# Kernel optimization log

Hardware: AMD Instinct MI355X
Metric: run time of the kernel (lower is better)

Reference implementation:

```python
import jax, jax.numpy as jnp
import numpy as np

S, D, H, L, FF = 4096, 128, 4, 3, 1024
DH = D // H
LN_EPS = 1e-5


def _layernorm(x, g, b):
    m = jnp.mean(x, axis=-1, keepdims=True)
    v = jnp.mean((x - m) ** 2, axis=-1, keepdims=True)
    return (x - m) * jax.lax.rsqrt(v + LN_EPS) * g + b


def setup_inputs() -> dict:
    key = jax.random.key(0)
    ks = jax.random.split(key, 16)
    w = lambda k, shp, s=0.05: jax.random.normal(k, shp, dtype=jnp.float32) * s
    return {
        "src": jax.random.normal(ks[0], (S, 1, D), dtype=jnp.float32),
        # per-layer transformer params, stacked on leading L axis
        "Wqkv": w(ks[1], (L, 3 * D, D)),
        "bqkv": jnp.zeros((L, 3 * D), jnp.float32),
        "Wo": w(ks[2], (L, D, D)),
        "bo": jnp.zeros((L, D), jnp.float32),
        "ln1_g": jnp.ones((L, D), jnp.float32),
        "ln1_b": jnp.zeros((L, D), jnp.float32),
        "W1": w(ks[3], (L, FF, D)),
        "b1": jnp.zeros((L, FF), jnp.float32),
        "W2": w(ks[4], (L, D, FF)),
        "b2": jnp.zeros((L, D), jnp.float32),
        "ln2_g": jnp.ones((L, D), jnp.float32),
        "ln2_b": jnp.zeros((L, D), jnp.float32),
        "fc1_W": w(ks[5], (D, D)),
        "fc1_b": jnp.zeros((D,), jnp.float32),
        "fc2_W": w(ks[6], (D, D)),
        "fc2_b": jnp.zeros((D,), jnp.float32),
    }


def reference(src, Wqkv, bqkv, Wo, bo, ln1_g, ln1_b, W1, b1, W2, b2,
              ln2_g, ln2_b, fc1_W, fc1_b, fc2_W, fc2_b):
    x = src[:, 0, :]  # [S, D] (batch=1, squeezed as in the torch module)
    scale = 1.0 / np.sqrt(DH).astype(np.float32)
    for l in range(L):  # small fixed layer count
        # --- self-attention (post-norm, as in torch TransformerEncoderLayer, eval mode) ---
        qkv = x @ Wqkv[l].T + bqkv[l]                      # [S, 3D]
        q, k, v = jnp.split(qkv, 3, axis=-1)
        q = q.reshape(S, H, DH)
        k = k.reshape(S, H, DH)
        v = v.reshape(S, H, DH)
        att = jax.nn.softmax(jnp.einsum('shd,thd->hst', q, k) * scale, axis=-1)
        o = jnp.einsum('hst,thd->shd', att, v).reshape(S, D)
        o = o @ Wo[l].T + bo[l]
        x = _layernorm(x + o, ln1_g[l], ln1_b[l])
        # --- feed-forward ---
        f = jax.nn.relu(x @ W1[l].T + b1[l]) @ W2[l].T + b2[l]
        x = _layernorm(x + f, ln2_g[l], ln2_b[l])
    # head
    x = jax.nn.relu(x @ fc1_W.T + fc1_b)
    x = x @ fc2_W.T + fc2_b
    # pairwise cosine similarity, clamped at min 1e-6 (vectorized form of pCosineSim)
    xn = x / jnp.linalg.norm(x, axis=1, keepdims=True)
    return jnp.maximum(xn @ xn.T, 1e-6)
```

## Files before the change

kernel.cpp:

```cpp
#include <hip/hip_runtime.h>
#include <math.h>

#define S 4096
#define QK_SCALE 0.17677669529663687f
#define LOG2E    1.44269504088896f
#define SPLIT 8
#define KS (S / SPLIT)

typedef _Float16 f16x8 __attribute__((ext_vector_type(8)));
typedef _Float16 f16x4 __attribute__((ext_vector_type(4)));
typedef _Float16 f16x2 __attribute__((ext_vector_type(2)));
typedef float f32x4 __attribute__((ext_vector_type(4)));

template<int R>
__device__ __forceinline__ void stageT(_Float16 (*dst)[136], const _Float16* __restrict__ src,
                                       int ld, int row0, int col0, int tid) {
    int r = tid >> 4, cb = (tid & 15) * 8;
#pragma unroll
    for (int v = 0; v < R / 16; v++)
        *(f16x8*)&dst[v * 16 + r][cb] =
            *(const f16x8*)(src + (size_t)(row0 + v * 16 + r) * ld + col0 + cb);
}

__global__ __launch_bounds__(256) void setup_cvt(const float* __restrict__ q,
                                                 const float* __restrict__ wo,
                                                 const float* __restrict__ w1,
                                                 const float* __restrict__ w2,
                                                 const float* __restrict__ f1,
                                                 const float* __restrict__ f2,
                                                 _Float16* __restrict__ dst,
                                                 const float* __restrict__ a,
                                                 float* __restrict__ x,
                                                 _Float16* __restrict__ xh)
{
    int bb = blockIdx.x;
    if (bb < 992) {
        const float* src; size_t dof; int lb;
        if (bb < 144)      { src = q;  dof = 0;      lb = bb; }
        else if (bb < 192) { src = wo; dof = 147456; lb = bb - 144; }
        else if (bb < 576) { src = w1; dof = 196608; lb = bb - 192; }
        else if (bb < 960) { src = w2; dof = 589824; lb = bb - 576; }
        else if (bb < 976) { src = f1; dof = 983040; lb = bb - 960; }
        else               { src = f2; dof = 999424; lb = bb - 976; }
        int i = lb * 1024 + threadIdx.x * 4;
        float4 v = *(const float4*)(src + i);
        f16x4 h = {(_Float16)v.x, (_Float16)v.y, (_Float16)v.z, (_Float16)v.w};
        *(f16x4*)(dst + dof + i) = h;
    } else {
        int i = (bb - 992) * 256 + threadIdx.x;
        float4 v = ((const float4*)a)[i];
        ((float4*)x)[i] = v;
        f16x4 h = {(_Float16)v.x, (_Float16)v.y, (_Float16)v.z, (_Float16)v.w};
        ((f16x4*)xh)[i] = h;
    }
}

__global__ __launch_bounds__(256) void gemm_qkv(const _Float16* __restrict__ xh,
                                                const _Float16* __restrict__ Wh,
                                                const float* __restrict__ bias,
                                                _Float16* __restrict__ qh,
                                                _Float16* __restrict__ kh,
                                                _Float16* __restrict__ vt)
{
    __shared__ _Float16 Ah[16][136], Bh[128][136];
    int tid = threadIdx.x, w = tid >> 6, l = tid & 63, lc = l & 15, lr = l >> 4;
    int m0 = blockIdx.x * 16, by = blockIdx.y;

    stageT<16>(Ah, xh, 128, m0, 0, tid);
    stageT<128>(Bh, Wh, 128, by * 128, 0, tid);
    __syncthreads();

    f32x4 acc[2];
#pragma unroll
    for (int j = 0; j < 2; j++) acc[j] = {0.f, 0.f, 0.f, 0.f};
#pragma unroll
    for (int ks = 0; ks < 4; ks++) {
        f16x8 af = *(const f16x8*)&Ah[lc][ks * 32 + lr * 8];
#pragma unroll
        for (int j = 0; j < 2; j++) {
            f16x8 bf = *(const f16x8*)&Bh[w * 32 + j * 16 + lc][ks * 32 + lr * 8];
            acc[j] = __builtin_amdgcn_mfma_f32_16x16x32_f16(af, bf, acc[j], 0, 0, 0);
        }
    }

    int mb = m0 + lr * 4;
#pragma unroll
    for (int j = 0; j < 2; j++) {
        int n = w * 32 + j * 16 + lc;
        float bb = bias[by * 128 + n];
        if (by == 0) {
#pragma unroll
            for (int r = 0; r < 4; r++)
                qh[(size_t)(mb + r) * 128 + n] =
                    (_Float16)((acc[j][r] + bb) * (QK_SCALE * LOG2E));
        } else if (by == 1) {
            int hh = n >> 5, d = n & 31;
#pragma unroll
            for (int r = 0; r < 4; r++)
                kh[((size_t)hh * S + mb + r) * 32 + d] = (_Float16)(acc[j][r] + bb);
        } else {
            f16x4 pk;
#pragma unroll
            for (int r = 0; r < 4; r++) pk[r] = (_Float16)(acc[j][r] + bb);
            *(f16x4*)&vt[(size_t)n * S + mb] = pk;
        }
    }
}

__global__ __launch_bounds__(256) void attn_mfma(const _Float16* __restrict__ qh,
                                                 const _Float16* __restrict__ kh,
                                                 const _Float16* __restrict__ vt,
                                                 _Float16* __restrict__ part,
                                                 float* __restrict__ mll)
{
    __shared__ _Float16 Ks[2][64][32];
    __shared__ _Float16 Vt[2][32][72];
    __shared__ _Float16 Ps[4][16][72];
    int h = blockIdx.y, q0 = blockIdx.x * 64, z = blockIdx.z;
    int tid = threadIdx.x;
    int w = tid >> 6, l = tid & 63;
    int lc = l & 15, lr = l >> 4;

    f16x8 qf = *(const f16x8*)&qh[(size_t)(q0 + w * 16 + lc) * 128 + h * 32 + lr * 8];

    const _Float16* khh = kh + (size_t)h * S * 32;
    const _Float16* vth = vt + (size_t)h * 32 * S;

    int krow = tid >> 2, kcol = (tid & 3) * 8;
    int vrow = tid >> 3, vcol = (tid & 7) * 8;

    f32x4 o0 = {0.f, 0.f, 0.f, 0.f}, o1 = {0.f, 0.f, 0.f, 0.f};
    float lp = 0.f;

    int k0 = z * KS;
    {
        f16x8 kr = *(const f16x8*)&khh[(size_t)(k0 + krow) * 32 + kcol];
        f16x8 vr = *(const f16x8*)&vth[(size_t)vrow * S + k0 + vcol];
        *(f16x8*)&Ks[0][krow][kcol] = kr;
        *(f16x8*)&Vt[0][vrow][vcol] = vr;
    }
    __syncthreads();

    int cur = 0;
#pragma unroll 1
    for (int t8 = 0; t8 < KS / 64; t8++) {
        bool more = (t8 + 1 < KS / 64);
        f16x8 kr, vr;
        if (more) {
            int kn = k0 + (t8 + 1) * 64;
            kr = *(const f16x8*)&khh[(size_t)(kn + krow) * 32 + kcol];
            vr = *(const f16x8*)&vth[(size_t)vrow * S + kn + vcol];
        }

        f32x4 st[4];
#pragma unroll
        for (int t = 0; t < 4; t++) {
            f16x8 kf = *(const f16x8*)&Ks[cur][t * 16 + lc][lr * 8];
            f32x4 zz = {0.f, 0.f, 0.f, 0.f};
            st[t] = __builtin_amdgcn_mfma_f32_16x16x32_f16(kf, qf, zz, 0, 0, 0);
        }
#pragma unroll
        for (int t = 0; t < 4; t++) {
            float p0 = exp2f(st[t][0]), p1 = exp2f(st[t][1]);
            float p2 = exp2f(st[t][2]), p3 = exp2f(st[t][3]);
            lp += (p0 + p1) + (p2 + p3);
            f16x2 h0 = {(_Float16)p0, (_Float16)p1};
            f16x2 h1 = {(_Float16)p2, (_Float16)p3};
            *(f16x2*)&Ps[w][lc][t * 16 + lr * 4]     = h0;
            *(f16x2*)&Ps[w][lc][t * 16 + lr * 4 + 2] = h1;
        }
        asm volatile("s_waitcnt lgkmcnt(0)" ::: "memory");
#pragma unroll
        for (int ch = 0; ch < 2; ch++) {
            f16x8 pf = *(const f16x8*)&Ps[w][lc][ch * 32 + lr * 8];
            f16x8 v0 = *(const f16x8*)&Vt[cur][lc][ch * 32 + lr * 8];
            f16x8 v1 = *(const f16x8*)&Vt[cur][16 + lc][ch * 32 + lr * 8];
            o0 = __builtin_amdgcn_mfma_f32_16x16x32_f16(pf, v0, o0, 0, 0, 0);
            o1 = __builtin_amdgcn_mfma_f32_16x16x32_f16(pf, v1, o1, 0, 0, 0);
        }
        if (more) {
            *(f16x8*)&Ks[cur ^ 1][krow][kcol] = kr;
            *(f16x8*)&Vt[cur ^ 1][vrow][vcol] = vr;
            __syncthreads();
        }
        cur ^= 1;
    }

    lp += __shfl_xor(lp, 16);
    lp += __shfl_xor(lp, 32);

    _Float16* pz = part + (size_t)z * 524288;
#pragma unroll
    for (int i = 0; i < 4; i++) {
        int q = q0 + w * 16 + lr * 4 + i;
        pz[(size_t)q * 128 + h * 32 + lc]      = (_Float16)o0[i];
        pz[(size_t)q * 128 + h * 32 + 16 + lc] = (_Float16)o1[i];
    }
    if (l < 16) mll[((size_t)z * 4 + h) * 4096 + q0 + w * 16 + lc] = lp;
}

__global__ __launch_bounds__(256) void wo_ln_merge(const _Float16* __restrict__ part,
                                                   const float* __restrict__ mll,
                                                   const _Float16* __restrict__ Wh,
                                                   const float* __restrict__ bias,
                                                   float* __restrict__ x,
                                                   _Float16* __restrict__ xh,
                                                   const float* __restrict__ g,
                                                   const float* __restrict__ b)
{
    __shared__ _Float16 Ah[16][136], Bh[128][136];
    __shared__ float Red[16][4][2];
    int tid = threadIdx.x, w = tid >> 6, l = tid & 63, lc = l & 15, lr = l >> 4;
    int m0 = blockIdx.x * 16;

    {
        int row = tid >> 4, col0 = (tid & 15) * 8;
        int q = m0 + row, hh = col0 >> 5;
        float lsum = 0.f;
#pragma unroll
        for (int s = 0; s < SPLIT; s++) lsum += mll[((size_t)s * 4 + hh) * 4096 + q];
        float am[8];
#pragma unroll
        for (int e = 0; e < 8; e++) am[e] = 0.f;
#pragma unroll
        for (int s = 0; s < SPLIT; s++) {
            f16x8 t = *(const f16x8*)&part[(size_t)s * 524288 + (size_t)q * 128 + col0];
#pragma unroll
            for (int e = 0; e < 8; e++) am[e] += (float)t[e];
        }
        float inv = 1.f / lsum;
        f16x8 hv;
#pragma unroll
        for (int e = 0; e < 8; e++) hv[e] = (_Float16)(am[e] * inv);
        *(f16x8*)&Ah[row][col0] = hv;
    }
    stageT<128>(Bh, Wh, 128, 0, 0, tid);
    __syncthreads();

    f32x4 acc[2];
#pragma unroll
    for (int j = 0; j < 2; j++) acc[j] = {0.f, 0.f, 0.f, 0.f};
#pragma unroll
    for (int ks = 0; ks < 4; ks++) {
        f16x8 af = *(const f16x8*)&Ah[lc][ks * 32 + lr * 8];
#pragma unroll
        for (int j = 0; j < 2; j++) {
            f16x8 bf = *(const f16x8*)&Bh[w * 32 + j * 16 + lc][ks * 32 + lr * 8];
            acc[j] = __builtin_amdgcn_mfma_f32_16x16x32_f16(af, bf, acc[j], 0, 0, 0);
        }
    }

#pragma unroll
    for (int j = 0; j < 2; j++) {
        int n = w * 32 + j * 16 + lc;
        float bb = bias[n];
#pragma unroll
        for (int r = 0; r < 4; r++)
            acc[j][r] += bb + x[(size_t)(m0 + lr * 4 + r) * 128 + n];
    }
#pragma unroll
    for (int r = 0; r < 4; r++) {
        float s1 = acc[0][r] + acc[1][r];
        float s2 = acc[0][r] * acc[0][r] + acc[1][r] * acc[1][r];
#pragma unroll
        for (int off = 1; off < 16; off <<= 1) {
            s1 += __shfl_xor(s1, off);
            s2 += __shfl_xor(s2, off);
        }
        if (lc == 0) { Red[lr * 4 + r][w][0] = s1; Red[lr * 4 + r][w][1] = s2; }
    }
    __syncthreads();
#pragma unroll
    for (int r = 0; r < 4; r++) {
        int rl = lr * 4 + r;
        float S1 = (Red[rl][0][0] + Red[rl][1][0]) + (Red[rl][2][0] + Red[rl][3][0]);
        float S2 = (Red[rl][0][1] + Red[rl][1][1]) + (Red[rl][2][1] + Red[rl][3][1]);
        float mean = S1 * (1.0f / 128.0f);
        float var = S2 * (1.0f / 128.0f) - mean * mean;
        float inv = rsqrtf(var + 1e-5f);
        int m = m0 + rl;
#pragma unroll
        for (int j = 0; j < 2; j++) {
            int n = w * 32 + j * 16 + lc;
            float o = (acc[j][r] - mean) * inv * g[n] + b[n];
            x[(size_t)m * 128 + n] = o;
            xh[(size_t)m * 128 + n] = (_Float16)o;
        }
    }
}

__global__ __launch_bounds__(256) void ffn_pair(const _Float16* __restrict__ xh,
                                                const _Float16* __restrict__ W1h,
                                                const float* __restrict__ b1,
                                                const _Float16* __restrict__ W2h,
                                                _Float16* __restrict__ wpart)
{
    __shared__ _Float16 Ah[64][136], Bh[128][136];
    int tid = threadIdx.x, w = tid >> 6, l = tid & 63, lc = l & 15, lr = l >> 4;
    int wr = w >> 1, wc = w & 1;
    int m0 = blockIdx.x * 64, c = blockIdx.y;

    stageT<64>(Ah, xh, 128, m0, 0, tid);
    stageT<128>(Bh, W1h, 128, c * 128, 0, tid);
    __syncthreads();

    f32x4 acc[2][4];
#pragma unroll
    for (int i = 0; i < 2; i++)
#pragma unroll
        for (int j = 0; j < 4; j++) acc[i][j] = {0.f, 0.f, 0.f, 0.f};
#pragma unroll
    for (int ks = 0; ks < 4; ks++) {
        f16x8 af0 = *(const f16x8*)&Ah[wr * 32 + lc][ks * 32 + lr * 8];
        f16x8 af1 = *(const f16x8*)&Ah[wr * 32 + 16 + lc][ks * 32 + lr * 8];
#pragma unroll
        for (int j = 0; j < 4; j++) {
            f16x8 bf = *(const f16x8*)&Bh[wc * 64 + j * 16 + lc][ks * 32 + lr * 8];
            acc[0][j] = __builtin_amdgcn_mfma_f32_16x16x32_f16(af0, bf, acc[0][j], 0, 0, 0);
            acc[1][j] = __builtin_amdgcn_mfma_f32_16x16x32_f16(af1, bf, acc[1][j], 0, 0, 0);
        }
    }
    __syncthreads();

#pragma unroll
    for (int i = 0; i < 2; i++)
#pragma unroll
        for (int j = 0; j < 4; j++) {
            int n = wc * 64 + j * 16 + lc;
            float bb = b1[c * 128 + n];
#pragma unroll
            for (int r = 0; r < 4; r++)
                Ah[wr * 32 + i * 16 + lr * 4 + r][n] =
                    (_Float16)fmaxf(acc[i][j][r] + bb, 0.f);
        }
    stageT<128>(Bh, W2h, 1024, 0, c * 128, tid);
    __syncthreads();

    f32x4 oacc[2][4];
#pragma unroll
    for (int i = 0; i < 2; i++)
#pragma unroll
        for (int j = 0; j < 4; j++) oacc[i][j] = {0.f, 0.f, 0.f, 0.f};
#pragma unroll
    for (int ks = 0; ks < 4; ks++) {
        f16x8 af0 = *(const f16x8*)&Ah[wr * 32 + lc][ks * 32 + lr * 8];
        f16x8 af1 = *(const f16x8*)&Ah[wr * 32 + 16 + lc][ks * 32 + lr * 8];
#pragma unroll
        for (int j = 0; j < 4; j++) {
            f16x8 bf = *(const f16x8*)&Bh[wc * 64 + j * 16 + lc][ks * 32 + lr * 8];
            oacc[0][j] = __builtin_amdgcn_mfma_f32_16x16x32_f16(af0, bf, oacc[0][j], 0, 0, 0);
            oacc[1][j] = __builtin_amdgcn_mfma_f32_16x16x32_f16(af1, bf, oacc[1][j], 0, 0, 0);
        }
    }

    _Float16* pz = wpart + (size_t)c * 524288;
#pragma unroll
    for (int i = 0; i < 2; i++) {
        int mb = m0 + wr * 32 + i * 16 + lr * 4;
#pragma unroll
        for (int j = 0; j < 4; j++) {
            int n = wc * 64 + j * 16 + lc;
#pragma unroll
            for (int r = 0; r < 4; r++)
                pz[(size_t)(mb + r) * 128 + n] = (_Float16)oacc[i][j][r];
        }
    }
}

__global__ __launch_bounds__(256) void reduce8_ln(const _Float16* __restrict__ part,
                                                  const float* __restrict__ bias,
                                                  float* __restrict__ x,
                                                  _Float16* __restrict__ xh,
                                                  const float* __restrict__ g,
                                                  const float* __restrict__ b)
{
    int row  = blockIdx.x * 4 + (threadIdx.x >> 6);
    int lane = threadIdx.x & 63;
    size_t base = (size_t)row * 128;
    int c = lane * 2;
    float a0 = 0.f, a1 = 0.f;
#pragma unroll
    for (int s = 0; s < 8; s++) {
        f16x2 p = *(const f16x2*)&part[(size_t)s * 524288 + base + c];
        a0 += (float)p[0]; a1 += (float)p[1];
    }
    float2 bv = *(const float2*)&bias[c];
    float2 xv = *(const float2*)&x[base + c];
    a0 += bv.x + xv.x; a1 += bv.y + xv.y;
    float s = a0 + a1;
#pragma unroll
    for (int off = 32; off; off >>= 1) s += __shfl_xor(s, off);
    float mean = s * (1.0f / 128.0f);
    float d0 = a0 - mean, d1 = a1 - mean;
    float v = d0 * d0 + d1 * d1;
#pragma unroll
    for (int off = 32; off; off >>= 1) v += __shfl_xor(v, off);
    float inv = rsqrtf(v * (1.0f / 128.0f) + 1e-5f);
    float2 gv = *(const float2*)&g[c];
    float2 bb = *(const float2*)&b[c];
    float o0 = d0 * inv * gv.x + bb.x, o1 = d1 * inv * gv.y + bb.y;
    float2 r; r.x = o0; r.y = o1;
    *(float2*)&x[base + c] = r;
    f16x2 rh = {(_Float16)o0, (_Float16)o1};
    *(f16x2*)&xh[base + c] = rh;
}

__global__ __launch_bounds__(256) void fc_fused(const _Float16* __restrict__ xh,
                                                const _Float16* __restrict__ W1h,
                                                const float* __restrict__ b1f,
                                                const _Float16* __restrict__ W2h,
                                                const float* __restrict__ b2f,
                                                _Float16* __restrict__ aoh)
{
    __shared__ _Float16 Ah[16][136], Bh[128][136];
    __shared__ float Red[16][4];
    int tid = threadIdx.x, w = tid >> 6, l = tid & 63, lc = l & 15, lr = l >> 4;
    int m0 = blockIdx.x * 16;

    stageT<16>(Ah, xh, 128, m0, 0, tid);
    stageT<128>(Bh, W1h, 128, 0, 0, tid);
    __syncthreads();

    f32x4 acc[2];
#pragma unroll
    for (int j = 0; j < 2; j++) acc[j] = {0.f, 0.f, 0.f, 0.f};
#pragma unroll
    for (int ks = 0; ks < 4; ks++) {
        f16x8 af = *(const f16x8*)&Ah[lc][ks * 32 + lr * 8];
#pragma unroll
        for (int j = 0; j < 2; j++) {
            f16x8 bf = *(const f16x8*)&Bh[w * 32 + j * 16 + lc][ks * 32 + lr * 8];
            acc[j] = __builtin_amdgcn_mfma_f32_16x16x32_f16(af, bf, acc[j], 0, 0, 0);
        }
    }
    __syncthreads();
#pragma unroll
    for (int j = 0; j < 2; j++) {
        int n = w * 32 + j * 16 + lc;
        float bb = b1f[n];
#pragma unroll
        for (int r = 0; r < 4; r++)
            Ah[lr * 4 + r][n] = (_Float16)fmaxf(acc[j][r] + bb, 0.f);
    }
    stageT<128>(Bh, W2h, 128, 0, 0, tid);
    __syncthreads();

    f32x4 o[2];
#pragma unroll
    for (int j = 0; j < 2; j++) o[j] = {0.f, 0.f, 0.f, 0.f};
#pragma unroll
    for (int ks = 0; ks < 4; ks++) {
        f16x8 af = *(const f16x8*)&Ah[lc][ks * 32 + lr * 8];
#pragma unroll
        for (int j = 0; j < 2; j++) {
            f16x8 bf = *(const f16x8*)&Bh[w * 32 + j * 16 + lc][ks * 32 + lr * 8];
            o[j] = __builtin_amdgcn_mfma_f32_16x16x32_f16(af, bf, o[j], 0, 0, 0);
        }
    }
#pragma unroll
    for (int j = 0; j < 2; j++) {
        float bb = b2f[w * 32 + j * 16 + lc];
#pragma unroll
        for (int r = 0; r < 4; r++) o[j][r] += bb;
    }
#pragma unroll
    for (int r = 0; r < 4; r++) {
        float s2 = o[0][r] * o[0][r] + o[1][r] * o[1][r];
#pragma unroll
        for (int off = 1; off < 16; off <<= 1) s2 += __shfl_xor(s2, off);
        if (lc == 0) Red[lr * 4 + r][w] = s2;
    }
    __syncthreads();
#pragma unroll
    for (int r = 0; r < 4; r++) {
        int rl = lr * 4 + r;
        float inv = rsqrtf((Red[rl][0] + Red[rl][1]) + (Red[rl][2] + Red[rl][3]));
        int m = m0 + rl;
#pragma unroll
        for (int j = 0; j < 2; j++) {
            int n = w * 32 + j * 16 + lc;
            aoh[(size_t)m * 128 + n] = (_Float16)(o[j][r] * inv);
        }
    }
}

__global__ __launch_bounds__(256) void gram_f16(const _Float16* __restrict__ aoh,
                                                float* __restrict__ C)
{
    __shared__ _Float16 Ah[64][136], Bh[128][136];
    int tid = threadIdx.x, w = tid >> 6, l = tid & 63, lc = l & 15, lr = l >> 4;
    int wr = w >> 1, wc = w & 1;
    int m0 = blockIdx.x * 64, n0 = blockIdx.y * 128;

    stageT<64>(Ah, aoh, 128, m0, 0, tid);
    stageT<128>(Bh, aoh, 128, n0, 0, tid);
    __syncthreads();

    f32x4 acc[2][4];
#pragma unroll
    for (int i = 0; i < 2; i++)
#pragma unroll
        for (int j = 0; j < 4; j++) acc[i][j] = {0.f, 0.f, 0.f, 0.f};
#pragma unroll
    for (int ks = 0; ks < 4; ks++) {
        f16x8 af0 = *(const f16x8*)&Ah[wr * 32 + lc][ks * 32 + lr * 8];
        f16x8 af1 = *(const f16x8*)&Ah[wr * 32 + 16 + lc][ks * 32 + lr * 8];
#pragma unroll
        for (int j = 0; j < 4; j++) {
            f16x8 bf = *(const f16x8*)&Bh[wc * 64 + j * 16 + lc][ks * 32 + lr * 8];
            acc[0][j] = __builtin_amdgcn_mfma_f32_16x16x32_f16(af0, bf, acc[0][j], 0, 0, 0);
            acc[1][j] = __builtin_amdgcn_mfma_f32_16x16x32_f16(af1, bf, acc[1][j], 0, 0, 0);
        }
    }

#pragma unroll
    for (int i = 0; i < 2; i++) {
        int mb = m0 + wr * 32 + i * 16 + lr * 4;
#pragma unroll
        for (int j = 0; j < 4; j++) {
            int n = n0 + wc * 64 + j * 16 + lc;
#pragma unroll
            for (int r = 0; r < 4; r++)
                C[(size_t)(mb + r) * 4096 + n] = fmaxf(acc[i][j][r], 1e-6f);
        }
    }
}

extern "C" void kernel_launch(void* const* d_in, const int* in_sizes, int n_in,
                              void* d_out, int out_size, void* d_ws, size_t ws_size,
                              hipStream_t stream)
{
    const float* src  = (const float*)d_in[0];
    const float* Wqkv = (const float*)d_in[1];
    const float* bqkv = (const float*)d_in[2];
    const float* Wo   = (const float*)d_in[3];
    const float* bo   = (const float*)d_in[4];
    const float* ln1g = (const float*)d_in[5];
    const float* ln1b = (const float*)d_in[6];
    const float* W1   = (const float*)d_in[7];
    const float* b1   = (const float*)d_in[8];
    const float* W2   = (const float*)d_in[9];
    const float* b2   = (const float*)d_in[10];
    const float* ln2g = (const float*)d_in[11];
    const float* ln2b = (const float*)d_in[12];
    const float* fc1W = (const float*)d_in[13];
    const float* fc1b = (const float*)d_in[14];
    const float* fc2W = (const float*)d_in[15];
    const float* fc2b = (const float*)d_in[16];

    float* ws = (float*)d_ws;
    float*    x   = ws;
    _Float16* xh  = (_Float16*)(ws + 524288);
    _Float16* aoh = (_Float16*)(ws + 786432);
    _Float16* qh  = (_Float16*)(ws + 1048576);
    _Float16* kh  = (_Float16*)(ws + 1310720);
    _Float16* vt  = (_Float16*)(ws + 1572864);
    float*    mll = ws + 1835008;

    _Float16* wpart = (_Float16*)d_out + 4194304;
    _Float16* apart = (_Float16*)d_out + 12582912;
    _Float16* wh    = (_Float16*)d_out + 16777216;
    float*    out   = (float*)d_out;

    _Float16* qkvh = wh;
    _Float16* woh  = wh + 147456;
    _Float16* w1h  = wh + 196608;
    _Float16* w2h  = wh + 589824;
    _Float16* fc1h = wh + 983040;
    _Float16* fc2h = wh + 999424;

    setup_cvt<<<1504, 256, 0, stream>>>(Wqkv, Wo, W1, W2, fc1W, fc2W, wh,
                                        src, x, xh);
    for (int l = 0; l < 3; l++) {
        gemm_qkv<<<dim3(256, 3), 256, 0, stream>>>(xh, qkvh + l * 49152,
                                                   bqkv + l * 384, qh, kh, vt);
        attn_mfma<<<dim3(64, 4, SPLIT), 256, 0, stream>>>(qh, kh, vt, apart, mll);
        wo_ln_merge<<<256, 256, 0, stream>>>(apart, mll, woh + l * 16384, bo + l * 128,
                                             x, xh, ln1g + l * 128, ln1b + l * 128);
        ffn_pair<<<dim3(64, 8), 256, 0, stream>>>(xh, w1h + l * 131072, b1 + l * 1024,
                                                  w2h + l * 131072, wpart);
        reduce8_ln<<<1024, 256, 0, stream>>>(wpart, b2 + l * 128, x, xh,
                                             ln2g + l * 128, ln2b + l * 128);
    }
    fc_fused<<<256, 256, 0, stream>>>(xh, fc1h, fc1b, fc2h, fc2b, aoh);
    gram_f16<<<dim3(64, 32), 256, 0, stream>>>(aoh, out);
}
```

Measured before the change: 263.3 us.

## Fuse Wo+LN1+FFN+LN2 into one layer_tail kernel, halve attention split, add setprio

Replaces the wo_ln_merge, ffn_pair and reduce8_ln kernels with a single per-16-row layer_tail kernel. It does the attention merge, the Wo projection, LN1, the full FFN with register-prefetched double-buffered weight tiles, and LN2, so the FFN partial-sum round trip through global memory and two launches disappear. The attention key split is cut from 8 to 4 and the MFMA sections get s_setprio hints. In exchange, each block now streams the full 256K fp16 FFN weights with only 256 blocks, which limits parallelism, and uses more LDS per block.

```diff
diff --git a/kernel.cpp b/kernel.cpp
--- a/kernel.cpp
+++ b/kernel.cpp
@@ -4,7 +4,7 @@
 #define S 4096
 #define QK_SCALE 0.17677669529663687f
 #define LOG2E    1.44269504088896f
-#define SPLIT 8
+#define SPLIT 4
 #define KS (S / SPLIT)
 
 typedef _Float16 f16x8 __attribute__((ext_vector_type(8)));
@@ -20,6 +20,20 @@
     for (int v = 0; v < R / 16; v++)
         *(f16x8*)&dst[v * 16 + r][cb] =
             *(const f16x8*)(src + (size_t)(row0 + v * 16 + r) * ld + col0 + cb);
+}
+
+__device__ __forceinline__ void ldT128(f16x8 pf[8], const _Float16* __restrict__ src,
+                                       int ld, int row0, int col0, int tid) {
+    int r = tid >> 4, cb = (tid & 15) * 8;
+#pragma unroll
+    for (int v = 0; v < 8; v++)
+        pf[v] = *(const f16x8*)(src + (size_t)(row0 + v * 16 + r) * ld + col0 + cb);
+}
+__device__ __forceinline__ void stT128(_Float16 (*dst)[136], const f16x8 pf[8], int tid) {
+    int r = tid >> 4, cb = (tid & 15) * 8;
+#pragma unroll
+    for (int v = 0; v < 8; v++)
+        *(f16x8*)&dst[v * 16 + r][cb] = pf[v];
 }
 
 __global__ __launch_bounds__(256) void setup_cvt(const float* __restrict__ q,
@@ -153,12 +167,14 @@
         }
 
         f32x4 st[4];
+        __builtin_amdgcn_s_setprio(1);
 #pragma unroll
         for (int t = 0; t < 4; t++) {
             f16x8 kf = *(const f16x8*)&Ks[cur][t * 16 + lc][lr * 8];
             f32x4 zz = {0.f, 0.f, 0.f, 0.f};
             st[t] = __builtin_amdgcn_mfma_f32_16x16x32_f16(kf, qf, zz, 0, 0, 0);
         }
+        __builtin_amdgcn_s_setprio(0);
 #pragma unroll
         for (int t = 0; t < 4; t++) {
             float p0 = exp2f(st[t][0]), p1 = exp2f(st[t][1]);
@@ -170,6 +186,7 @@
             *(f16x2*)&Ps[w][lc][t * 16 + lr * 4 + 2] = h1;
         }
         asm volatile("s_waitcnt lgkmcnt(0)" ::: "memory");
+        __builtin_amdgcn_s_setprio(1);
 #pragma unroll
         for (int ch = 0; ch < 2; ch++) {
             f16x8 pf = *(const f16x8*)&Ps[w][lc][ch * 32 + lr * 8];
@@ -178,6 +195,7 @@
             o0 = __builtin_amdgcn_mfma_f32_16x16x32_f16(pf, v0, o0, 0, 0, 0);
             o1 = __builtin_amdgcn_mfma_f32_16x16x32_f16(pf, v1, o1, 0, 0, 0);
         }
+        __builtin_amdgcn_s_setprio(0);
         if (more) {
             *(f16x8*)&Ks[cur ^ 1][krow][kcol] = kr;
             *(f16x8*)&Vt[cur ^ 1][vrow][vcol] = vr;
@@ -199,16 +217,24 @@
     if (l < 16) mll[((size_t)z * 4 + h) * 4096 + q0 + w * 16 + lc] = lp;
 }
 
-__global__ __launch_bounds__(256) void wo_ln_merge(const _Float16* __restrict__ part,
-                                                   const float* __restrict__ mll,
-                                                   const _Float16* __restrict__ Wh,
-                                                   const float* __restrict__ bias,
-                                                   float* __restrict__ x,
-                                                   _Float16* __restrict__ xh,
-                                                   const float* __restrict__ g,
-                                                   const float* __restrict__ b)
-{
-    __shared__ _Float16 Ah[16][136], Bh[128][136];
+__global__ __launch_bounds__(256) void layer_tail(const _Float16* __restrict__ part,
+                                                  const float* __restrict__ mll,
+                                                  const _Float16* __restrict__ Woh,
+                                                  const float* __restrict__ bo,
+                                                  const _Float16* __restrict__ W1h,
+                                                  const float* __restrict__ b1,
+                                                  const _Float16* __restrict__ W2h,
+                                                  const float* __restrict__ b2,
+                                                  const float* __restrict__ g1,
+                                                  const float* __restrict__ bn1,
+                                                  const float* __restrict__ g2,
+                                                  const float* __restrict__ bn2,
+                                                  float* __restrict__ x,
+                                                  _Float16* __restrict__ xh)
+{
+    __shared__ _Float16 Ah[16][136];
+    __shared__ _Float16 Bh[2][128][136];
+    __shared__ _Float16 Fh[16][1032];
     __shared__ float Red[16][4][2];
     int tid = threadIdx.x, w = tid >> 6, l = tid & 63, lc = l & 15, lr = l >> 4;
     int m0 = blockIdx.x * 16;
@@ -234,8 +260,15 @@
         for (int e = 0; e < 8; e++) hv[e] = (_Float16)(am[e] * inv);
         *(f16x8*)&Ah[row][col0] = hv;
     }
-    stageT<128>(Bh, Wh, 128, 0, 0, tid);
-    __syncthreads();
+    stageT<128>(Bh[0], Woh, 128, 0, 0, tid);
+    __syncthreads();
+
+    float xv[2][4];
+#pragma unroll
+    for (int j = 0; j < 2; j++)
+#pragma unroll
+        for (int r = 0; r < 4; r++)
+            xv[j][r] = x[(size_t)(m0 + lr * 4 + r) * 128 + w * 32 + j * 16 + lc];
 
     f32x4 acc[2];
 #pragma unroll
@@ -245,23 +278,116 @@
         f16x8 af = *(const f16x8*)&Ah[lc][ks * 32 + lr * 8];
 #pragma unroll
         for (int j = 0; j < 2; j++) {
-            f16x8 bf = *(const f16x8*)&Bh[w * 32 + j * 16 + lc][ks * 32 + lr * 8];
+            f16x8 bf = *(const f16x8*)&Bh[0][w * 32 + j * 16 + lc][ks * 32 + lr * 8];
             acc[j] = __builtin_amdgcn_mfma_f32_16x16x32_f16(af, bf, acc[j], 0, 0, 0);
         }
     }
+
+    f16x8 pf[8];
+    ldT128(pf, W1h, 128, 0, 0, tid);
 
 #pragma unroll
     for (int j = 0; j < 2; j++) {
         int n = w * 32 + j * 16 + lc;
-        float bb = bias[n];
-#pragma unroll
-        for (int r = 0; r < 4; r++)
-            acc[j][r] += bb + x[(size_t)(m0 + lr * 4 + r) * 128 + n];
+        float bb = bo[n];
+#pragma unroll
+        for (int r = 0; r < 4; r++) acc[j][r] += bb + xv[j][r];
     }
 #pragma unroll
     for (int r = 0; r < 4; r++) {
         float s1 = acc[0][r] + acc[1][r];
         float s2 = acc[0][r] * acc[0][r] + acc[1][r] * acc[1][r];
+#pragma unroll
+        for (int off = 1; off < 16; off <<= 1) {
+            s1 += __shfl_xor(s1, off);
+            s2 += __shfl_xor(s2, off);
+        }
+        if (lc == 0) { Red[lr * 4 + r][w][0] = s1; Red[lr * 4 + r][w][1] = s2; }
+    }
+    __syncthreads();
+
+    float ln1v[2][4];
+#pragma unroll
+    for (int r = 0; r < 4; r++) {
+        int rl = lr * 4 + r;
+        float S1 = (Red[rl][0][0] + Red[rl][1][0]) + (Red[rl][2][0] + Red[rl][3][0]);
+        float S2 = (Red[rl][0][1] + Red[rl][1][1]) + (Red[rl][2][1] + Red[rl][3][1]);
+        float mean = S1 * (1.0f / 128.0f);
+        float var = S2 * (1.0f / 128.0f) - mean * mean;
+        float inv = rsqrtf(var + 1e-5f);
+#pragma unroll
+        for (int j = 0; j < 2; j++) {
+            int n = w * 32 + j * 16 + lc;
+            ln1v[j][r] = (acc[j][r] - mean) * inv * g1[n] + bn1[n];
+            Ah[rl][n] = (_Float16)ln1v[j][r];
+        }
+    }
+    stT128(Bh[1], pf, tid);
+    __syncthreads();
+
+    int cur = 1;
+#pragma unroll 1
+    for (int c = 0; c < 8; c++) {
+        if (c < 7) ldT128(pf, W1h, 128, (c + 1) * 128, 0, tid);
+        else       ldT128(pf, W2h, 1024, 0, 0, tid);
+        f32x4 fa[2];
+#pragma unroll
+        for (int j = 0; j < 2; j++) fa[j] = {0.f, 0.f, 0.f, 0.f};
+#pragma unroll
+        for (int ks = 0; ks < 4; ks++) {
+            f16x8 af = *(const f16x8*)&Ah[lc][ks * 32 + lr * 8];
+#pragma unroll
+            for (int j = 0; j < 2; j++) {
+                f16x8 bf = *(const f16x8*)&Bh[cur][w * 32 + j * 16 + lc][ks * 32 + lr * 8];
+                fa[j] = __builtin_amdgcn_mfma_f32_16x16x32_f16(af, bf, fa[j], 0, 0, 0);
+            }
+        }
+#pragma unroll
+        for (int j = 0; j < 2; j++) {
+            int n = w * 32 + j * 16 + lc;
+            float bb = b1[c * 128 + n];
+#pragma unroll
+            for (int r = 0; r < 4; r++)
+                Fh[lr * 4 + r][c * 128 + n] = (_Float16)fmaxf(fa[j][r] + bb, 0.f);
+        }
+        stT128(Bh[cur ^ 1], pf, tid);
+        __syncthreads();
+        cur ^= 1;
+    }
+
+    f32x4 oacc[2];
+#pragma unroll
+    for (int j = 0; j < 2; j++) oacc[j] = {0.f, 0.f, 0.f, 0.f};
+#pragma unroll 1
+    for (int c = 0; c < 8; c++) {
+        if (c < 7) ldT128(pf, W2h, 1024, 0, (c + 1) * 128, tid);
+#pragma unroll
+        for (int ks = 0; ks < 4; ks++) {
+            f16x8 af = *(const f16x8*)&Fh[lc][c * 128 + ks * 32 + lr * 8];
+#pragma unroll
+            for (int j = 0; j < 2; j++) {
+                f16x8 bf = *(const f16x8*)&Bh[cur][w * 32 + j * 16 + lc][ks * 32 + lr * 8];
+                oacc[j] = __builtin_amdgcn_mfma_f32_16x16x32_f16(af, bf, oacc[j], 0, 0, 0);
+            }
+        }
+        if (c < 7) {
+            stT128(Bh[cur ^ 1], pf, tid);
+            __syncthreads();
+            cur ^= 1;
+        }
+    }
+
+#pragma unroll
+    for (int j = 0; j < 2; j++) {
+        int n = w * 32 + j * 16 + lc;
+        float bb = b2[n];
+#pragma unroll
+        for (int r = 0; r < 4; r++) oacc[j][r] += bb + ln1v[j][r];
+    }
+#pragma unroll
+    for (int r = 0; r < 4; r++) {
+        float s1 = oacc[0][r] + oacc[1][r];
+        float s2 = oacc[0][r] * oacc[0][r] + oacc[1][r] * oacc[1][r];
 #pragma unroll
         for (int off = 1; off < 16; off <<= 1) {
             s1 += __shfl_xor(s1, off);
@@ -282,127 +408,11 @@
 #pragma unroll
         for (int j = 0; j < 2; j++) {
             int n = w * 32 + j * 16 + lc;
-            float o = (acc[j][r] - mean) * inv * g[n] + b[n];
+            float o = (oacc[j][r] - mean) * inv * g2[n] + bn2[n];
             x[(size_t)m * 128 + n] = o;
             xh[(size_t)m * 128 + n] = (_Float16)o;
         }
     }
-}
-
-__global__ __launch_bounds__(256) void ffn_pair(const _Float16* __restrict__ xh,
-                                                const _Float16* __restrict__ W1h,
-                                                const float* __restrict__ b1,
-                                                const _Float16* __restrict__ W2h,
-                                                _Float16* __restrict__ wpart)
-{
-    __shared__ _Float16 Ah[64][136], Bh[128][136];
-    int tid = threadIdx.x, w = tid >> 6, l = tid & 63, lc = l & 15, lr = l >> 4;
-    int wr = w >> 1, wc = w & 1;
-    int m0 = blockIdx.x * 64, c = blockIdx.y;
-
-    stageT<64>(Ah, xh, 128, m0, 0, tid);
-    stageT<128>(Bh, W1h, 128, c * 128, 0, tid);
-    __syncthreads();
-
-    f32x4 acc[2][4];
-#pragma unroll
-    for (int i = 0; i < 2; i++)
-#pragma unroll
-        for (int j = 0; j < 4; j++) acc[i][j] = {0.f, 0.f, 0.f, 0.f};
-#pragma unroll
-    for (int ks = 0; ks < 4; ks++) {
-        f16x8 af0 = *(const f16x8*)&Ah[wr * 32 + lc][ks * 32 + lr * 8];
-        f16x8 af1 = *(const f16x8*)&Ah[wr * 32 + 16 + lc][ks * 32 + lr * 8];
-#pragma unroll
-        for (int j = 0; j < 4; j++) {
-            f16x8 bf = *(const f16x8*)&Bh[wc * 64 + j * 16 + lc][ks * 32 + lr * 8];
-            acc[0][j] = __builtin_amdgcn_mfma_f32_16x16x32_f16(af0, bf, acc[0][j], 0, 0, 0);
-            acc[1][j] = __builtin_amdgcn_mfma_f32_16x16x32_f16(af1, bf, acc[1][j], 0, 0, 0);
-        }
-    }
-    __syncthreads();
-
-#pragma unroll
-    for (int i = 0; i < 2; i++)
-#pragma unroll
-        for (int j = 0; j < 4; j++) {
-            int n = wc * 64 + j * 16 + lc;
-            float bb = b1[c * 128 + n];
-#pragma unroll
-            for (int r = 0; r < 4; r++)
-                Ah[wr * 32 + i * 16 + lr * 4 + r][n] =
-                    (_Float16)fmaxf(acc[i][j][r] + bb, 0.f);
-        }
-    stageT<128>(Bh, W2h, 1024, 0, c * 128, tid);
-    __syncthreads();
-
-    f32x4 oacc[2][4];
-#pragma unroll
-    for (int i = 0; i < 2; i++)
-#pragma unroll
-        for (int j = 0; j < 4; j++) oacc[i][j] = {0.f, 0.f, 0.f, 0.f};
-#pragma unroll
-    for (int ks = 0; ks < 4; ks++) {
-        f16x8 af0 = *(const f16x8*)&Ah[wr * 32 + lc][ks * 32 + lr * 8];
-        f16x8 af1 = *(const f16x8*)&Ah[wr * 32 + 16 + lc][ks * 32 + lr * 8];
-#pragma unroll
-        for (int j = 0; j < 4; j++) {
-            f16x8 bf = *(const f16x8*)&Bh[wc * 64 + j * 16 + lc][ks * 32 + lr * 8];
-            oacc[0][j] = __builtin_amdgcn_mfma_f32_16x16x32_f16(af0, bf, oacc[0][j], 0, 0, 0);
-            oacc[1][j] = __builtin_amdgcn_mfma_f32_16x16x32_f16(af1, bf, oacc[1][j], 0, 0, 0);
-        }
-    }
-
-    _Float16* pz = wpart + (size_t)c * 524288;
-#pragma unroll
-    for (int i = 0; i < 2; i++) {
-        int mb = m0 + wr * 32 + i * 16 + lr * 4;
-#pragma unroll
-        for (int j = 0; j < 4; j++) {
-            int n = wc * 64 + j * 16 + lc;
-#pragma unroll
-            for (int r = 0; r < 4; r++)
-                pz[(size_t)(mb + r) * 128 + n] = (_Float16)oacc[i][j][r];
-        }
-    }
-}
-
-__global__ __launch_bounds__(256) void reduce8_ln(const _Float16* __restrict__ part,
-                                                  const float* __restrict__ bias,
-                                                  float* __restrict__ x,
-                                                  _Float16* __restrict__ xh,
-                                                  const float* __restrict__ g,
-                                                  const float* __restrict__ b)
-{
-    int row  = blockIdx.x * 4 + (threadIdx.x >> 6);
-    int lane = threadIdx.x & 63;
-    size_t base = (size_t)row * 128;
-    int c = lane * 2;
-    float a0 = 0.f, a1 = 0.f;
-#pragma unroll
-    for (int s = 0; s < 8; s++) {
-        f16x2 p = *(const f16x2*)&part[(size_t)s * 524288 + base + c];
-        a0 += (float)p[0]; a1 += (float)p[1];
-    }
-    float2 bv = *(const float2*)&bias[c];
-    float2 xv = *(const float2*)&x[base + c];
-    a0 += bv.x + xv.x; a1 += bv.y + xv.y;
-    float s = a0 + a1;
-#pragma unroll
-    for (int off = 32; off; off >>= 1) s += __shfl_xor(s, off);
-    float mean = s * (1.0f / 128.0f);
-    float d0 = a0 - mean, d1 = a1 - mean;
-    float v = d0 * d0 + d1 * d1;
-#pragma unroll
-    for (int off = 32; off; off >>= 1) v += __shfl_xor(v, off);
-    float inv = rsqrtf(v * (1.0f / 128.0f) + 1e-5f);
-    float2 gv = *(const float2*)&g[c];
-    float2 bb = *(const float2*)&b[c];
-    float o0 = d0 * inv * gv.x + bb.x, o1 = d1 * inv * gv.y + bb.y;
-    float2 r; r.x = o0; r.y = o1;
-    *(float2*)&x[base + c] = r;
-    f16x2 rh = {(_Float16)o0, (_Float16)o1};
-    *(f16x2*)&xh[base + c] = rh;
 }
 
 __global__ __launch_bounds__(256) void fc_fused(const _Float16* __restrict__ xh,
@@ -557,7 +567,6 @@
     _Float16* vt  = (_Float16*)(ws + 1572864);
     float*    mll = ws + 1835008;
 
-    _Float16* wpart = (_Float16*)d_out + 4194304;
     _Float16* apart = (_Float16*)d_out + 12582912;
     _Float16* wh    = (_Float16*)d_out + 16777216;
     float*    out   = (float*)d_out;
@@ -575,12 +584,11 @@
         gemm_qkv<<<dim3(256, 3), 256, 0, stream>>>(xh, qkvh + l * 49152,
                                                    bqkv + l * 384, qh, kh, vt);
         attn_mfma<<<dim3(64, 4, SPLIT), 256, 0, stream>>>(qh, kh, vt, apart, mll);
-        wo_ln_merge<<<256, 256, 0, stream>>>(apart, mll, woh + l * 16384, bo + l * 128,
-                                             x, xh, ln1g + l * 128, ln1b + l * 128);
-        ffn_pair<<<dim3(64, 8), 256, 0, stream>>>(xh, w1h + l * 131072, b1 + l * 1024,
-                                                  w2h + l * 131072, wpart);
-        reduce8_ln<<<1024, 256, 0, stream>>>(wpart, b2 + l * 128, x, xh,
-                                             ln2g + l * 128, ln2b + l * 128);
+        layer_tail<<<256, 256, 0, stream>>>(apart, mll, woh + l * 16384, bo + l * 128,
+                                            w1h + l * 131072, b1 + l * 1024,
+                                            w2h + l * 131072, b2 + l * 128,
+                                            ln1g + l * 128, ln1b + l * 128,
+                                            ln2g + l * 128, ln2b + l * 128, x, xh);
     }
     fc_fused<<<256, 256, 0, stream>>>(xh, fc1h, fc1b, fc2h, fc2b, aoh);
     gram_f16<<<dim3(64, 32), 256, 0, stream>>>(aoh, out);
```

Result: slower. 272.4 us (+3.5%).

## Process two query tiles per attention block to reuse staged K/V tiles

Applied to the files above, without the earlier changes.

Each attention block now handles 128 queries instead of 64, running the QK^T, exp and PV steps twice per staged K/V tile so each K/V load from global memory and LDS serves two query groups. The V fragments are held in registers across both halves, and the grid is halved in x. A launch-bounds occupancy hint is added. The cost is higher register pressure and fewer blocks (1024), which could reduce latency hiding. Reusing the per-wave P buffer also serialises the two halves.

```diff
diff --git a/kernel.cpp b/kernel.cpp
--- a/kernel.cpp
+++ b/kernel.cpp
@@ -107,21 +107,22 @@
     }
 }
 
-__global__ __launch_bounds__(256) void attn_mfma(const _Float16* __restrict__ qh,
-                                                 const _Float16* __restrict__ kh,
-                                                 const _Float16* __restrict__ vt,
-                                                 _Float16* __restrict__ part,
-                                                 float* __restrict__ mll)
+__global__ __launch_bounds__(256, 4) void attn_mfma(const _Float16* __restrict__ qh,
+                                                    const _Float16* __restrict__ kh,
+                                                    const _Float16* __restrict__ vt,
+                                                    _Float16* __restrict__ part,
+                                                    float* __restrict__ mll)
 {
     __shared__ _Float16 Ks[2][64][32];
     __shared__ _Float16 Vt[2][32][72];
     __shared__ _Float16 Ps[4][16][72];
-    int h = blockIdx.y, q0 = blockIdx.x * 64, z = blockIdx.z;
+    int h = blockIdx.y, q0 = blockIdx.x * 128, z = blockIdx.z;
     int tid = threadIdx.x;
     int w = tid >> 6, l = tid & 63;
     int lc = l & 15, lr = l >> 4;
 
-    f16x8 qf = *(const f16x8*)&qh[(size_t)(q0 + w * 16 + lc) * 128 + h * 32 + lr * 8];
+    f16x8 qfa = *(const f16x8*)&qh[(size_t)(q0 + w * 16 + lc) * 128 + h * 32 + lr * 8];
+    f16x8 qfb = *(const f16x8*)&qh[(size_t)(q0 + 64 + w * 16 + lc) * 128 + h * 32 + lr * 8];
 
     const _Float16* khh = kh + (size_t)h * S * 32;
     const _Float16* vth = vt + (size_t)h * 32 * S;
@@ -129,8 +130,9 @@
     int krow = tid >> 2, kcol = (tid & 3) * 8;
     int vrow = tid >> 3, vcol = (tid & 7) * 8;
 
-    f32x4 o0 = {0.f, 0.f, 0.f, 0.f}, o1 = {0.f, 0.f, 0.f, 0.f};
-    float lp = 0.f;
+    f32x4 oa0 = {0.f, 0.f, 0.f, 0.f}, oa1 = {0.f, 0.f, 0.f, 0.f};
+    f32x4 ob0 = {0.f, 0.f, 0.f, 0.f}, ob1 = {0.f, 0.f, 0.f, 0.f};
+    float lpa = 0.f, lpb = 0.f;
 
     int k0 = z * KS;
     {
@@ -157,27 +159,58 @@
         for (int t = 0; t < 4; t++) {
             f16x8 kf = *(const f16x8*)&Ks[cur][t * 16 + lc][lr * 8];
             f32x4 zz = {0.f, 0.f, 0.f, 0.f};
-            st[t] = __builtin_amdgcn_mfma_f32_16x16x32_f16(kf, qf, zz, 0, 0, 0);
+            st[t] = __builtin_amdgcn_mfma_f32_16x16x32_f16(kf, qfa, zz, 0, 0, 0);
         }
 #pragma unroll
         for (int t = 0; t < 4; t++) {
             float p0 = exp2f(st[t][0]), p1 = exp2f(st[t][1]);
             float p2 = exp2f(st[t][2]), p3 = exp2f(st[t][3]);
-            lp += (p0 + p1) + (p2 + p3);
+            lpa += (p0 + p1) + (p2 + p3);
             f16x2 h0 = {(_Float16)p0, (_Float16)p1};
             f16x2 h1 = {(_Float16)p2, (_Float16)p3};
             *(f16x2*)&Ps[w][lc][t * 16 + lr * 4]     = h0;
             *(f16x2*)&Ps[w][lc][t * 16 + lr * 4 + 2] = h1;
         }
         asm volatile("s_waitcnt lgkmcnt(0)" ::: "memory");
-#pragma unroll
-        for (int ch = 0; ch < 2; ch++) {
-            f16x8 pf = *(const f16x8*)&Ps[w][lc][ch * 32 + lr * 8];
-            f16x8 v0 = *(const f16x8*)&Vt[cur][lc][ch * 32 + lr * 8];
-            f16x8 v1 = *(const f16x8*)&Vt[cur][16 + lc][ch * 32 + lr * 8];
-            o0 = __builtin_amdgcn_mfma_f32_16x16x32_f16(pf, v0, o0, 0, 0, 0);
-            o1 = __builtin_amdgcn_mfma_f32_16x16x32_f16(pf, v1, o1, 0, 0, 0);
-        }
+        f16x8 vg0 = *(const f16x8*)&Vt[cur][lc][lr * 8];
+        f16x8 vg1 = *(const f16x8*)&Vt[cur][16 + lc][lr * 8];
+        f16x8 vg2 = *(const f16x8*)&Vt[cur][lc][32 + lr * 8];
+        f16x8 vg3 = *(const f16x8*)&Vt[cur][16 + lc][32 + lr * 8];
+        {
+            f16x8 pf0 = *(const f16x8*)&Ps[w][lc][lr * 8];
+            f16x8 pf1 = *(const f16x8*)&Ps[w][lc][32 + lr * 8];
+            oa0 = __builtin_amdgcn_mfma_f32_16x16x32_f16(pf0, vg0, oa0, 0, 0, 0);
+            oa1 = __builtin_amdgcn_mfma_f32_16x16x32_f16(pf0, vg1, oa1, 0, 0, 0);
+            oa0 = __builtin_amdgcn_mfma_f32_16x16x32_f16(pf1, vg2, oa0, 0, 0, 0);
+            oa1 = __builtin_amdgcn_mfma_f32_16x16x32_f16(pf1, vg3, oa1, 0, 0, 0);
+        }
+
+#pragma unroll
+        for (int t = 0; t < 4; t++) {
+            f16x8 kf = *(const f16x8*)&Ks[cur][t * 16 + lc][lr * 8];
+            f32x4 zz = {0.f, 0.f, 0.f, 0.f};
+            st[t] = __builtin_amdgcn_mfma_f32_16x16x32_f16(kf, qfb, zz, 0, 0, 0);
+        }
+#pragma unroll
+        for (int t = 0; t < 4; t++) {
+            float p0 = exp2f(st[t][0]), p1 = exp2f(st[t][1]);
+            float p2 = exp2f(st[t][2]), p3 = exp2f(st[t][3]);
+            lpb += (p0 + p1) + (p2 + p3);
+            f16x2 h0 = {(_Float16)p0, (_Float16)p1};
+            f16x2 h1 = {(_Float16)p2, (_Float16)p3};
+            *(f16x2*)&Ps[w][lc][t * 16 + lr * 4]     = h0;
+            *(f16x2*)&Ps[w][lc][t * 16 + lr * 4 + 2] = h1;
+        }
+        asm volatile("s_waitcnt lgkmcnt(0)" ::: "memory");
+        {
+            f16x8 pf0 = *(const f16x8*)&Ps[w][lc][lr * 8];
+            f16x8 pf1 = *(const f16x8*)&Ps[w][lc][32 + lr * 8];
+            ob0 = __builtin_amdgcn_mfma_f32_16x16x32_f16(pf0, vg0, ob0, 0, 0, 0);
+            ob1 = __builtin_amdgcn_mfma_f32_16x16x32_f16(pf0, vg1, ob1, 0, 0, 0);
+            ob0 = __builtin_amdgcn_mfma_f32_16x16x32_f16(pf1, vg2, ob0, 0, 0, 0);
+            ob1 = __builtin_amdgcn_mfma_f32_16x16x32_f16(pf1, vg3, ob1, 0, 0, 0);
+        }
+
         if (more) {
             *(f16x8*)&Ks[cur ^ 1][krow][kcol] = kr;
             *(f16x8*)&Vt[cur ^ 1][vrow][vcol] = vr;
@@ -186,17 +219,25 @@
         cur ^= 1;
     }
 
-    lp += __shfl_xor(lp, 16);
-    lp += __shfl_xor(lp, 32);
+    lpa += __shfl_xor(lpa, 16);
+    lpa += __shfl_xor(lpa, 32);
+    lpb += __shfl_xor(lpb, 16);
+    lpb += __shfl_xor(lpb, 32);
 
     _Float16* pz = part + (size_t)z * 524288;
 #pragma unroll
     for (int i = 0; i < 4; i++) {
-        int q = q0 + w * 16 + lr * 4 + i;
-        pz[(size_t)q * 128 + h * 32 + lc]      = (_Float16)o0[i];
-        pz[(size_t)q * 128 + h * 32 + 16 + lc] = (_Float16)o1[i];
-    }
-    if (l < 16) mll[((size_t)z * 4 + h) * 4096 + q0 + w * 16 + lc] = lp;
+        int qa = q0 + w * 16 + lr * 4 + i;
+        int qb = qa + 64;
+        pz[(size_t)qa * 128 + h * 32 + lc]      = (_Float16)oa0[i];
+        pz[(size_t)qa * 128 + h * 32 + 16 + lc] = (_Float16)oa1[i];
+        pz[(size_t)qb * 128 + h * 32 + lc]      = (_Float16)ob0[i];
+        pz[(size_t)qb * 128 + h * 32 + 16 + lc] = (_Float16)ob1[i];
+    }
+    if (l < 16) {
+        mll[((size_t)z * 4 + h) * 4096 + q0 + w * 16 + lc]      = lpa;
+        mll[((size_t)z * 4 + h) * 4096 + q0 + 64 + w * 16 + lc] = lpb;
+    }
 }
 
 __global__ __launch_bounds__(256) void wo_ln_merge(const _Float16* __restrict__ part,
@@ -574,7 +615,7 @@
     for (int l = 0; l < 3; l++) {
         gemm_qkv<<<dim3(256, 3), 256, 0, stream>>>(xh, qkvh + l * 49152,
                                                    bqkv + l * 384, qh, kh, vt);
-        attn_mfma<<<dim3(64, 4, SPLIT), 256, 0, stream>>>(qh, kh, vt, apart, mll);
+        attn_mfma<<<dim3(32, 4, SPLIT), 256, 0, stream>>>(qh, kh, vt, apart, mll);
         wo_ln_merge<<<256, 256, 0, stream>>>(apart, mll, woh + l * 16384, bo + l * 128,
                                              x, xh, ln1g + l * 128, ln1b + l * 128);
         ffn_pair<<<dim3(64, 8), 256, 0, stream>>>(xh, w1h + l * 131072, b1 + l * 1024,
```

Measured after the change: 271.1 us. 2.9% more time.
